# Performance work log

Hardware: AMD Instinct MI355X
Metric: run time of the kernel (lower is better)

Reference implementation:

```python
import jax, jax.numpy as jnp
import numpy as np

D, N = 512, 65536


def setup_inputs() -> dict:
    key = jax.random.key(0)
    k1, k2 = jax.random.split(key)
    feats = jax.random.normal(k1, (D, N), dtype=jnp.float32)
    warped_feats = jax.random.normal(k2, (D, N), dtype=jnp.float32)
    return {"feats": feats, "warped_feats": warped_feats}


def reference(feats, warped_feats):
    # diag(feats.T @ warped_feats)[n] == sum_d feats[d,n] * warped_feats[d,n]
    # Same math as the torch module, without materializing the NxN matrix.
    diag = jnp.einsum('dn,dn->n', feats, warped_feats)  # [N]
    cosine = 1.0 - diag
    return cosine.mean()
```

## Files before the change

### kernel.cpp

```cpp
#include <hip/hip_runtime.h>

#define THREADS 512
#define BLOCKS  1024
#define ITERS   16
#define UNROLL  4

typedef float f32x4 __attribute__((ext_vector_type(4)));

__global__ __launch_bounds__(THREADS) void dot_partial_kernel(
        const f32x4* __restrict__ a,
        const f32x4* __restrict__ b,
        float* __restrict__ partial) {
    const int base = blockIdx.x * (ITERS * THREADS) + threadIdx.x;

    f32x4 acc0 = (f32x4)0.f, acc1 = (f32x4)0.f, acc2 = (f32x4)0.f, acc3 = (f32x4)0.f;

    #pragma unroll
    for (int i = 0; i < ITERS; i += UNROLL) {
        const int i0 = base + (i + 0) * THREADS;
        const int i1 = base + (i + 1) * THREADS;
        const int i2 = base + (i + 2) * THREADS;
        const int i3 = base + (i + 3) * THREADS;
        f32x4 a0 = a[i0];
        f32x4 b0 = b[i0];
        f32x4 a1 = a[i1];
        f32x4 b1 = b[i1];
        f32x4 a2 = a[i2];
        f32x4 b2 = b[i2];
        f32x4 a3 = a[i3];
        f32x4 b3 = b[i3];
        acc0 += a0 * b0;
        acc1 += a1 * b1;
        acc2 += a2 * b2;
        acc3 += a3 * b3;
    }

    f32x4 accv = (acc0 + acc1) + (acc2 + acc3);
    float s = (accv.x + accv.y) + (accv.z + accv.w);

    #pragma unroll
    for (int off = 32; off > 0; off >>= 1)
        s += __shfl_down(s, off, 64);

    __shared__ float smem[THREADS / 64];
    const int lane = threadIdx.x & 63;
    const int wave = threadIdx.x >> 6;
    if (lane == 0) smem[wave] = s;
    __syncthreads();

    if (threadIdx.x == 0) {
        float t = 0.f;
        #pragma unroll
        for (int w = 0; w < THREADS / 64; ++w) t += smem[w];
        partial[blockIdx.x] = t;
    }
}

__global__ __launch_bounds__(256) void final_reduce_kernel(
        const float* __restrict__ partial,
        float* __restrict__ out,
        int np, float inv_n) {
    float s = 0.f;
    for (int i = threadIdx.x; i < np; i += 256) s += partial[i];

    #pragma unroll
    for (int off = 32; off > 0; off >>= 1)
        s += __shfl_down(s, off, 64);

    __shared__ float smem[4];
    const int lane = threadIdx.x & 63;
    const int wave = threadIdx.x >> 6;
    if (lane == 0) smem[wave] = s;
    __syncthreads();

    if (threadIdx.x == 0) {
        float t = 0.f;
        #pragma unroll
        for (int w = 0; w < 4; ++w) t += smem[w];
        out[0] = 1.0f - t * inv_n;
    }
}

extern "C" void kernel_launch(void* const* d_in, const int* in_sizes, int n_in,
                              void* d_out, int out_size, void* d_ws, size_t ws_size,
                              hipStream_t stream) {
    const float* feats  = (const float*)d_in[0];
    const float* warped = (const float*)d_in[1];
    float* out = (float*)d_out;
    float* ws  = (float*)d_ws;

    const float inv_n = 1.0f / 65536.0f;

    dot_partial_kernel<<<BLOCKS, THREADS, 0, stream>>>(
        (const f32x4*)feats, (const f32x4*)warped, ws);
    final_reduce_kernel<<<1, 256, 0, stream>>>(ws, out, BLOCKS, inv_n);
}
```

Baseline: 279.5 us.

## Stream inputs through per-wave double-buffered LDS via global_load_lds

Replaces direct vectorized global loads with per-wave double-buffered asynchronous global-to-LDS copies (global_load_lds, 16 bytes per lane), using vmcnt waits so the next chunk loads while the current one is consumed. Block shape changes to 256 threads by 2048 blocks, with each wave processing a contiguous chunk. The aim is to keep memory requests in flight on a purely bandwidth-bound dot product. It gives up the previous 8 independent loads in flight per thread, since only about one stage is prefetched ahead, and it adds an LDS round trip.

```diff
diff --git a/kernel.cpp b/kernel.cpp
--- a/kernel.cpp
+++ b/kernel.cpp
@@ -1,57 +1,75 @@
 #include <hip/hip_runtime.h>
 
-#define THREADS 512
-#define BLOCKS  1024
+#define THREADS 256
+#define BLOCKS  2048
 #define ITERS   16
-#define UNROLL  4
 
 typedef float f32x4 __attribute__((ext_vector_type(4)));
 
+#define BUF_BYTES      2048
+#define WAVE_LDS_BYTES (2 * BUF_BYTES)
+
 __global__ __launch_bounds__(THREADS) void dot_partial_kernel(
-        const f32x4* __restrict__ a,
-        const f32x4* __restrict__ b,
+        const float* __restrict__ a,
+        const float* __restrict__ b,
         float* __restrict__ partial) {
-    const int base = blockIdx.x * (ITERS * THREADS) + threadIdx.x;
+    __shared__ __align__(16) char lds[4 * WAVE_LDS_BYTES];
+    __shared__ float smem_red[THREADS / 64];
 
-    f32x4 acc0 = (f32x4)0.f, acc1 = (f32x4)0.f, acc2 = (f32x4)0.f, acc3 = (f32x4)0.f;
+    const int wave = threadIdx.x >> 6;
+    const int lane = threadIdx.x & 63;
 
+    char* wbase = lds + wave * WAVE_LDS_BYTES;
+
+    const long long wchunk0 = ((long long)blockIdx.x * 4 + wave) * ITERS;
+
+    auto stage = [&](int i, int buf) {
+        const long long f4 = (wchunk0 + i) * 64 + lane;
+        const float* ga = a + f4 * 4;
+        const float* gb = b + f4 * 4;
+        char* la = wbase + buf * BUF_BYTES;
+        char* lb = la + 1024;
+        __builtin_amdgcn_global_load_lds(
+            (const __attribute__((address_space(1))) void*)ga,
+            (__attribute__((address_space(3))) void*)la, 16, 0, 0);
+        __builtin_amdgcn_global_load_lds(
+            (const __attribute__((address_space(1))) void*)gb,
+            (__attribute__((address_space(3))) void*)lb, 16, 0, 0);
+    };
+
+    f32x4 acc0 = (f32x4)0.f, acc1 = (f32x4)0.f;
+
+    stage(0, 0);
     #pragma unroll
-    for (int i = 0; i < ITERS; i += UNROLL) {
-        const int i0 = base + (i + 0) * THREADS;
-        const int i1 = base + (i + 1) * THREADS;
-        const int i2 = base + (i + 2) * THREADS;
-        const int i3 = base + (i + 3) * THREADS;
-        f32x4 a0 = a[i0];
-        f32x4 b0 = b[i0];
-        f32x4 a1 = a[i1];
-        f32x4 b1 = b[i1];
-        f32x4 a2 = a[i2];
-        f32x4 b2 = b[i2];
-        f32x4 a3 = a[i3];
-        f32x4 b3 = b[i3];
-        acc0 += a0 * b0;
-        acc1 += a1 * b1;
-        acc2 += a2 * b2;
-        acc3 += a3 * b3;
+    for (int i = 0; i < ITERS; ++i) {
+        const int buf = i & 1;
+        if (i + 1 < ITERS) {
+            stage(i + 1, buf ^ 1);
+            __asm__ volatile("s_waitcnt vmcnt(2)" ::: "memory");
+        } else {
+            __asm__ volatile("s_waitcnt vmcnt(0)" ::: "memory");
+        }
+        const char* la = wbase + buf * BUF_BYTES;
+        const char* lb = la + 1024;
+        f32x4 av = *(const f32x4*)(la + lane * 16);
+        f32x4 bv = *(const f32x4*)(lb + lane * 16);
+        if (buf) acc1 += av * bv; else acc0 += av * bv;
     }
 
-    f32x4 accv = (acc0 + acc1) + (acc2 + acc3);
+    f32x4 accv = acc0 + acc1;
     float s = (accv.x + accv.y) + (accv.z + accv.w);
 
     #pragma unroll
     for (int off = 32; off > 0; off >>= 1)
         s += __shfl_down(s, off, 64);
 
-    __shared__ float smem[THREADS / 64];
-    const int lane = threadIdx.x & 63;
-    const int wave = threadIdx.x >> 6;
-    if (lane == 0) smem[wave] = s;
+    if (lane == 0) smem_red[wave] = s;
     __syncthreads();
 
     if (threadIdx.x == 0) {
         float t = 0.f;
         #pragma unroll
-        for (int w = 0; w < THREADS / 64; ++w) t += smem[w];
+        for (int w = 0; w < THREADS / 64; ++w) t += smem_red[w];
         partial[blockIdx.x] = t;
     }
 }
@@ -91,7 +109,6 @@
 
     const float inv_n = 1.0f / 65536.0f;
 
-    dot_partial_kernel<<<BLOCKS, THREADS, 0, stream>>>(
-        (const f32x4*)feats, (const f32x4*)warped, ws);
+    dot_partial_kernel<<<BLOCKS, THREADS, 0, stream>>>(feats, warped, ws);
     final_reduce_kernel<<<1, 256, 0, stream>>>(ws, out, BLOCKS, inv_n);
 }
```

After: 275.7 us. No clear change (-1.4%).

## Software-pipeline nontemporal loads with smaller blocks and more of them

Applied to the files above, without the earlier changes.

Restructures the partial dot-product kernel into a rolling register pipeline that keeps six vector load pairs in flight, refilling each slot after it is consumed. The loads now use nontemporal hints to avoid polluting the cache with streaming data. Block size drops to 256 threads and block count doubles, with an occupancy hint in the launch bounds. The partial buffer grows to 2048 entries for the final reduction. This targets memory latency hiding in a purely bandwidth-bound stream, at the cost of more register pressure.

```diff
diff --git a/kernel.cpp b/kernel.cpp
--- a/kernel.cpp
+++ b/kernel.cpp
@@ -1,41 +1,40 @@
 #include <hip/hip_runtime.h>
 
-#define THREADS 512
-#define BLOCKS  1024
-#define ITERS   16
-#define UNROLL  4
+#define THREADS 256
+#define BLOCKS  2048
+#define CHUNKS  16
+#define PIPE    6
 
 typedef float f32x4 __attribute__((ext_vector_type(4)));
 
-__global__ __launch_bounds__(THREADS) void dot_partial_kernel(
+__global__ __launch_bounds__(THREADS, 8) void dot_partial_kernel(
         const f32x4* __restrict__ a,
         const f32x4* __restrict__ b,
         float* __restrict__ partial) {
-    const int base = blockIdx.x * (ITERS * THREADS) + threadIdx.x;
+    const int base = blockIdx.x * (CHUNKS * THREADS) + threadIdx.x;
 
-    f32x4 acc0 = (f32x4)0.f, acc1 = (f32x4)0.f, acc2 = (f32x4)0.f, acc3 = (f32x4)0.f;
+    f32x4 va[PIPE], vb[PIPE];
 
     #pragma unroll
-    for (int i = 0; i < ITERS; i += UNROLL) {
-        const int i0 = base + (i + 0) * THREADS;
-        const int i1 = base + (i + 1) * THREADS;
-        const int i2 = base + (i + 2) * THREADS;
-        const int i3 = base + (i + 3) * THREADS;
-        f32x4 a0 = a[i0];
-        f32x4 b0 = b[i0];
-        f32x4 a1 = a[i1];
-        f32x4 b1 = b[i1];
-        f32x4 a2 = a[i2];
-        f32x4 b2 = b[i2];
-        f32x4 a3 = a[i3];
-        f32x4 b3 = b[i3];
-        acc0 += a0 * b0;
-        acc1 += a1 * b1;
-        acc2 += a2 * b2;
-        acc3 += a3 * b3;
+    for (int i = 0; i < PIPE; ++i) {
+        va[i] = __builtin_nontemporal_load(a + base + i * THREADS);
+        vb[i] = __builtin_nontemporal_load(b + base + i * THREADS);
     }
 
-    f32x4 accv = (acc0 + acc1) + (acc2 + acc3);
+    f32x4 acc0 = (f32x4)0.f, acc1 = (f32x4)0.f;
+
+    #pragma unroll
+    for (int i = 0; i < CHUNKS; ++i) {
+        const int slot = i % PIPE;
+        if (i & 1) acc1 += va[slot] * vb[slot];
+        else       acc0 += va[slot] * vb[slot];
+        if (i + PIPE < CHUNKS) {
+            va[slot] = __builtin_nontemporal_load(a + base + (i + PIPE) * THREADS);
+            vb[slot] = __builtin_nontemporal_load(b + base + (i + PIPE) * THREADS);
+        }
+    }
+
+    f32x4 accv = acc0 + acc1;
     float s = (accv.x + accv.y) + (accv.z + accv.w);
 
     #pragma unroll
```

New measurement: 249.0 us. 10.9% less time.
